# Kernel optimization log

Hardware: AMD Instinct MI355X
Metric: run time of the kernel (lower is better)

Reference implementation:

```python
import jax, jax.numpy as jnp
import numpy as np
import math

N_HEAD = 16

def _rope_tables(seq, dh, dtype):
    inv_freq = 1.0 / (10000.0 ** (jnp.arange(0, dh, 2, dtype=jnp.float32) / dh))
    angle = jnp.arange(seq, dtype=jnp.float32)[:, None] * inv_freq[None, :]  # [S, dh/2]
    sin = jnp.repeat(jnp.sin(angle), 2, axis=-1).astype(dtype)  # [S, dh]
    cos = jnp.repeat(jnp.cos(angle), 2, axis=-1).astype(dtype)
    return sin, cos

def _rotate_half(x):
    x_even = x[..., ::2]
    x_odd = x[..., 1::2]
    return jnp.stack([-x_odd, x_even], axis=-1).reshape(x.shape)

def _apply_rope(x, sin, cos):
    # x: [B, H, S, dh]; sin/cos: [S, dh]
    return x * cos[None, None] + _rotate_half(x) * sin[None, None]

def setup_inputs() -> dict:
    key = jax.random.key(0)
    ks = jax.random.split(key, 9)
    B, S, D = 2, 2048, 2048
    scale = 1.0 / math.sqrt(D)
    x = jax.random.normal(ks[0], (B, S, D), dtype=jnp.float32)
    wq = jax.random.normal(ks[1], (D, D), dtype=jnp.float32) * scale
    wk = jax.random.normal(ks[2], (D, D), dtype=jnp.float32) * scale
    wv = jax.random.normal(ks[3], (D, D), dtype=jnp.float32) * scale
    wo = jax.random.normal(ks[4], (D, D), dtype=jnp.float32) * scale
    bq = jnp.zeros((D,), jnp.float32)
    bk = jnp.zeros((D,), jnp.float32)
    bv = jnp.zeros((D,), jnp.float32)
    bo = jnp.zeros((D,), jnp.float32)
    # causal mask: True = masked (strict upper triangle)
    mask = jnp.triu(jnp.ones((S, S), dtype=bool), k=1)[None, None]  # [1,1,S,S]
    return {"x": x, "wq": wq, "bq": bq, "wk": wk, "bk": bk, "wv": wv, "bv": bv,
            "wo": wo, "bo": bo, "mask": mask}

def reference(x, wq, bq, wk, bk, wv, bv, wo, bo, mask):
    B, S, D = x.shape
    H = N_HEAD
    dh = D // H
    # projections (torch Linear: x @ W.T + b)
    q = (x @ wq.T + bq).reshape(B, S, H, dh).transpose(0, 2, 1, 3)  # [B,H,S,dh]
    k = (x @ wk.T + bk).reshape(B, S, H, dh).transpose(0, 2, 1, 3)
    v = (x @ wv.T + bv).reshape(B, S, H, dh).transpose(0, 2, 1, 3)
    sin, cos = _rope_tables(S, dh, x.dtype)
    q = _apply_rope(q, sin, cos)
    k = _apply_rope(k, sin, cos)
    scores = jnp.einsum('bhqd,bhkd->bhqk', q, k) / math.sqrt(dh)
    scores = jnp.where(mask, -jnp.inf, scores)
    attn = jax.nn.softmax(scores, axis=-1)
    attn = jnp.nan_to_num(attn, nan=0.0)
    out = jnp.einsum('bhqk,bhkd->bhqd', attn, v)  # [B,H,S,dh]
    out = out.transpose(0, 2, 1, 3).reshape(B, S, D)
    return out @ wo.T + bo
```

## Files before the change

### kernel.cpp

```cpp
#include <hip/hip_runtime.h>
#include <math.h>


typedef _Float16 half8 __attribute__((ext_vector_type(8)));
typedef _Float16 half4v __attribute__((ext_vector_type(4)));
typedef float f32x4 __attribute__((ext_vector_type(4)));

__device__ __forceinline__ void gl_lds16(const void* g, void* l) {
  __builtin_amdgcn_global_load_lds(
      (const __attribute__((address_space(1))) unsigned int*)g,
      (__attribute__((address_space(3))) unsigned int*)l, 16, 0, 0);
}

__global__ void cast_f32_f16(const float* __restrict__ src, _Float16* __restrict__ dst, int n4) {
  int i = blockIdx.x * blockDim.x + threadIdx.x;
  if (i >= n4) return;
  float4 v = reinterpret_cast<const float4*>(src)[i];
  half4v o;
  o[0] = (_Float16)v.x; o[1] = (_Float16)v.y; o[2] = (_Float16)v.z; o[3] = (_Float16)v.w;
  reinterpret_cast<half4v*>(dst)[i] = o;
}

__global__ void cast_w(const float* __restrict__ w0, const float* __restrict__ w1,
                       const float* __restrict__ w2, const float* __restrict__ w3,
                       _Float16* __restrict__ wdst) {
  const float* s = blockIdx.y == 0 ? w0 : blockIdx.y == 1 ? w1 : blockIdx.y == 2 ? w2 : w3;
  int i = blockIdx.x * blockDim.x + threadIdx.x;
  float4 v = reinterpret_cast<const float4*>(s)[i];
  half4v o;
  o[0] = (_Float16)v.x; o[1] = (_Float16)v.y; o[2] = (_Float16)v.z; o[3] = (_Float16)v.w;
  reinterpret_cast<half4v*>(wdst)[(size_t)blockIdx.y * 1048576 + i] = o;
}

template <bool OUT_F32>
__global__ __launch_bounds__(512, 2) void gemm_bt256(
    const _Float16* __restrict__ A,
    const _Float16* __restrict__ B,
    const float* __restrict__ b0, const float* __restrict__ b1,
    const float* __restrict__ b2,
    void* __restrict__ Cout,
    int M, int N, int K) {
  __shared__ _Float16 As[2][16384];
  __shared__ _Float16 Bs[2][16384];
  const int bm = blockIdx.y * 256, bn = blockIdx.x * 256;
  const int tid = threadIdx.x;
  const int wave = tid >> 6, lane = tid & 63;
  const int quad = lane >> 4, l16 = lane & 15;
  const int wm = (wave >> 2) * 128, wn = (wave & 3) * 64;

  const int srow = tid >> 3;
  const int sx = (tid & 7) ^ (srow & 7);
  const _Float16* Ag = A + (size_t)(bm + srow) * K + sx * 8;
  const _Float16* Bg[4];
#pragma unroll
  for (int c = 0; c < 4; ++c) {
    int r = (((c * 2 + (srow >> 5)) & 3) << 6) + ((c >> 1) << 5) + (srow & 31);
    Bg[c] = B + (size_t)(bn + r) * K + sx * 8;
  }

#define STAGE_A(buf, R, kt) \
  gl_lds16(Ag + (size_t)(R) * K + (kt) * 64, &As[buf][(R) * 64 + tid * 8])
#define STAGE_B(buf, c, kt) \
  gl_lds16(Bg[c] + (kt) * 64, &Bs[buf][(c) * 4096 + tid * 8])

  const int axor = l16 & 7;
  const int sl0 = ((0 + quad) ^ axor) * 8;
  const int sl1 = ((4 + quad) ^ axor) * 8;
  const int aoff = (wm + l16) * 64;
  const int q4 = (wn >> 6) * 32;

#define RD_A(i, kk) \
  (*reinterpret_cast<const half8*>(&As[cur][aoff + (i) * 1024 + ((kk) ? sl1 : sl0)]))
#define RD_B(j, kk) \
  (*reinterpret_cast<const half8*>( \
      &Bs[cur][((((j) >> 1) * 128 + q4 + ((j) & 1) * 16 + l16)) * 64 + ((kk) ? sl1 : sl0)]))

  f32x4 acc[8][4];
#pragma unroll
  for (int i = 0; i < 8; ++i)
#pragma unroll
    for (int j = 0; j < 4; ++j) acc[i][j] = f32x4{0.f, 0.f, 0.f, 0.f};

  half8 a[4][2], b[4][2];
  const int NT = K >> 6;

  STAGE_A(0, 0, 0); STAGE_A(0, 128, 0);
  STAGE_B(0, 0, 0); STAGE_B(0, 1, 0);
  STAGE_B(0, 2, 0); STAGE_B(0, 3, 0);
  STAGE_A(0, 64, 0); STAGE_A(0, 192, 0);
  if (NT > 1) {
    STAGE_A(1, 0, 1); STAGE_A(1, 128, 1);
    STAGE_B(1, 0, 1); STAGE_B(1, 1, 1);
    STAGE_B(1, 2, 1); STAGE_B(1, 3, 1);
    asm volatile("s_waitcnt vmcnt(6)");
  } else {
    asm volatile("s_waitcnt vmcnt(0)");
  }
  __builtin_amdgcn_s_barrier();

  for (int t = 0; t < NT; ++t) {
    const int cur = t & 1, nxt = cur ^ 1;
    const bool pf1 = (t + 1 < NT);
    const bool pf2 = (t + 2 < NT);

#pragma unroll
    for (int i = 0; i < 4; ++i) {
      a[i][0] = RD_A(i, 0); a[i][1] = RD_A(i, 1);
    }
#pragma unroll
    for (int j = 0; j < 2; ++j) {
      b[j][0] = RD_B(j, 0); b[j][1] = RD_B(j, 1);
    }
    if (pf1) { STAGE_A(nxt, 64, t + 1); STAGE_A(nxt, 192, t + 1); }
    __builtin_amdgcn_s_barrier();
    __builtin_amdgcn_s_setprio(1);
#pragma unroll
    for (int i = 0; i < 4; ++i)
#pragma unroll
      for (int j = 0; j < 2; ++j) {
        acc[i][j] = __builtin_amdgcn_mfma_f32_16x16x32_f16(a[i][0], b[j][0], acc[i][j], 0, 0, 0);
        acc[i][j] = __builtin_amdgcn_mfma_f32_16x16x32_f16(a[i][1], b[j][1], acc[i][j], 0, 0, 0);
      }
    __builtin_amdgcn_s_setprio(0);
    __builtin_amdgcn_s_barrier();

#pragma unroll
    for (int j = 2; j < 4; ++j) {
      b[j][0] = RD_B(j, 0); b[j][1] = RD_B(j, 1);
    }
    if (pf2) { STAGE_A(cur, 0, t + 2); STAGE_A(cur, 128, t + 2); }
    __builtin_amdgcn_s_barrier();
    __builtin_amdgcn_s_setprio(1);
#pragma unroll
    for (int i = 0; i < 4; ++i)
#pragma unroll
      for (int j = 2; j < 4; ++j) {
        acc[i][j] = __builtin_amdgcn_mfma_f32_16x16x32_f16(a[i][0], b[j][0], acc[i][j], 0, 0, 0);
        acc[i][j] = __builtin_amdgcn_mfma_f32_16x16x32_f16(a[i][1], b[j][1], acc[i][j], 0, 0, 0);
      }
    __builtin_amdgcn_s_setprio(0);
    __builtin_amdgcn_s_barrier();

#pragma unroll
    for (int i = 0; i < 4; ++i) {
      a[i][0] = RD_A(i + 4, 0); a[i][1] = RD_A(i + 4, 1);
    }
    if (pf2) { STAGE_B(cur, 0, t + 2); STAGE_B(cur, 1, t + 2); }
    __builtin_amdgcn_s_barrier();
    __builtin_amdgcn_s_setprio(1);
#pragma unroll
    for (int i = 0; i < 4; ++i)
#pragma unroll
      for (int j = 0; j < 2; ++j) {
        acc[i + 4][j] = __builtin_amdgcn_mfma_f32_16x16x32_f16(a[i][0], b[j][0], acc[i + 4][j], 0, 0, 0);
        acc[i + 4][j] = __builtin_amdgcn_mfma_f32_16x16x32_f16(a[i][1], b[j][1], acc[i + 4][j], 0, 0, 0);
      }
    __builtin_amdgcn_s_setprio(0);
    __builtin_amdgcn_s_barrier();

    if (pf2) { STAGE_B(cur, 2, t + 2); STAGE_B(cur, 3, t + 2); }
    __builtin_amdgcn_s_barrier();
    __builtin_amdgcn_s_setprio(1);
#pragma unroll
    for (int i = 0; i < 4; ++i)
#pragma unroll
      for (int j = 2; j < 4; ++j) {
        acc[i + 4][j] = __builtin_amdgcn_mfma_f32_16x16x32_f16(a[i][0], b[j][0], acc[i + 4][j], 0, 0, 0);
        acc[i + 4][j] = __builtin_amdgcn_mfma_f32_16x16x32_f16(a[i][1], b[j][1], acc[i + 4][j], 0, 0, 0);
      }
    __builtin_amdgcn_s_setprio(0);
    if (pf2)
      asm volatile("s_waitcnt vmcnt(6)");
    else
      asm volatile("s_waitcnt vmcnt(0)");
    __builtin_amdgcn_s_barrier();
  }

#pragma unroll
  for (int j = 0; j < 4; ++j) {
    const int gc = bn + wn + j * 16 + l16;
    const float* bp = (gc < 2048) ? b0 : (gc < 4096 ? b1 : b2);
    const float bz = bp[gc & 2047];
#pragma unroll
    for (int i = 0; i < 8; ++i) {
#pragma unroll
      for (int r = 0; r < 4; ++r) {
        const int gr = bm + wm + i * 16 + quad * 4 + r;
        float v = acc[i][j][r] + bz;
        if (OUT_F32)
          reinterpret_cast<float*>(Cout)[(size_t)gr * N + gc] = v;
        else
          reinterpret_cast<_Float16*>(Cout)[(size_t)gr * N + gc] = (_Float16)v;
      }
    }
  }
#undef STAGE_A
#undef STAGE_B
#undef RD_A
#undef RD_B
}

__global__ void rope_inplace(_Float16* __restrict__ qkv, int ngroups) {
  int idx = blockIdx.x * blockDim.x + threadIdx.x;
  if (idx >= ngroups) return;
  int m = idx >> 8;
  int g = idx & 255;
  int s = m & 2047;
  const float scale = 0.088388347648318447f;
  size_t base = (size_t)m * 6144 + g * 8;
  half8 qv = *reinterpret_cast<const half8*>(qkv + base);
  half8 kv = *reinterpret_cast<const half8*>(qkv + base + 2048);
  half8 qo, ko;
#pragma unroll
  for (int j = 0; j < 4; ++j) {
    int i = (g * 4 + j) & 63;
    float ang = (float)s * exp2f(-0.2076205059304601f * (float)i);
    float sn, cs;
    __sincosf(ang, &sn, &cs);
    float e = (float)qv[j * 2], o = (float)qv[j * 2 + 1];
    qo[j * 2]     = (_Float16)((e * cs - o * sn) * scale);
    qo[j * 2 + 1] = (_Float16)((o * cs + e * sn) * scale);
    e = (float)kv[j * 2]; o = (float)kv[j * 2 + 1];
    ko[j * 2]     = (_Float16)(e * cs - o * sn);
    ko[j * 2 + 1] = (_Float16)(o * cs + e * sn);
  }
  *reinterpret_cast<half8*>(qkv + base) = qo;
  *reinterpret_cast<half8*>(qkv + base + 2048) = ko;
}

__global__ __launch_bounds__(256) void transpose_v(const _Float16* __restrict__ qkv,
                                                   _Float16* __restrict__ vt) {
  __shared__ _Float16 t[64][72];
  const int s0 = blockIdx.x * 64;
  const int d0 = blockIdx.y * 64;
  const int bh = blockIdx.z;
  const int b = bh >> 4, h = bh & 15;
  const int tid = threadIdx.x;
#pragma unroll
  for (int p = 0; p < 2; ++p) {
    int chunk = p * 256 + tid;
    int r = chunk >> 3, c8 = (chunk & 7) * 8;
    *reinterpret_cast<half8*>(&t[r][c8]) = *reinterpret_cast<const half8*>(
        &qkv[(size_t)(b * 2048 + s0 + r) * 6144 + 4096 + h * 128 + d0 + c8]);
  }
  __syncthreads();
#pragma unroll
  for (int p = 0; p < 2; ++p) {
    int chunk = p * 256 + tid;
    int dr = chunk >> 3, c8 = (chunk & 7) * 8;
    half8 o;
#pragma unroll
    for (int j = 0; j < 8; ++j) o[j] = t[c8 + j][dr];
    *reinterpret_cast<half8*>(&vt[(size_t)(bh * 128 + d0 + dr) * 2048 + s0 + c8]) = o;
  }
}

__global__ __launch_bounds__(256, 2) void attn_kernel(
    const _Float16* __restrict__ QKV,
    const _Float16* __restrict__ VT,
    _Float16* __restrict__ ctx) {
  constexpr int LD = 6144, S = 2048;
  __shared__ _Float16 Ks[2][8192];
  __shared__ _Float16 Vs[2][8192];
  __shared__ _Float16 P[4][16][80];
  const int bid = blockIdx.x;
  const int bh = bid & 31;
  const int idx = (bid >> 5) & 7;
  const int qb = (bid >> 8) ? idx : 15 - idx;
  const int b = bh >> 4, h = bh & 15;
  const int tid = threadIdx.x;
  const int wv = tid >> 6, lane = tid & 63;
  const int quad = lane >> 4, l16 = lane & 15;
  const int q0 = qb * 128 + wv * 16;
  const int NJ = 2 * qb + 2;

  const _Float16* qp0 = QKV + (size_t)(b * S + q0 + l16) * LD + h * 128;
  half8 aq0[4], aq1[4];
#pragma unroll
  for (int ks = 0; ks < 4; ++ks) {
    aq0[ks] = *reinterpret_cast<const half8*>(qp0 + ks * 32 + quad * 8);
    aq1[ks] = *reinterpret_cast<const half8*>(qp0 + (size_t)64 * LD + ks * 32 + quad * 8);
  }

  const _Float16* gk[4];
  const _Float16* gv[4];
  int lofs[4];
#pragma unroll
  for (int p = 0; p < 4; ++p) {
    int c = p * 256 + tid;
    int cs = c ^ ((c >> 3) & 7);
    int cl16 = cs & 15, cqd = (cs >> 4) & 3;
    int cks = (cs >> 6) & 3, cf = cs >> 8;
    gk[p] = QKV + (size_t)(b * S + cf * 16 + cl16) * LD + 2048 + h * 128 + cks * 32 + cqd * 8;
    int ckv = (cs >> 6) & 1, ct = cs >> 7;
    gv[p] = VT + (size_t)(bh * 128 + ct * 16 + cl16) * S + ckv * 32 + cqd * 8;
    lofs[p] = c * 8;
  }

  const int kofs = (l16 >> 3) * 64 + (((l16 & 7) ^ (quad * 2 + (l16 >> 3)))) * 8;

  f32x4 acc0[8], acc1[8];
#pragma unroll
  for (int t = 0; t < 8; ++t) {
    acc0[t] = f32x4{0.f, 0.f, 0.f, 0.f};
    acc1[t] = f32x4{0.f, 0.f, 0.f, 0.f};
  }
  f32x4 lacc0 = f32x4{0.f, 0.f, 0.f, 0.f};
  f32x4 lacc1 = f32x4{0.f, 0.f, 0.f, 0.f};

  half8 ones;
#pragma unroll
  for (int j = 0; j < 8; ++j) ones[j] = (_Float16)1.0f;

#pragma unroll
  for (int p = 0; p < 4; ++p) gl_lds16(gk[p], &Ks[0][lofs[p]]);
#pragma unroll
  for (int p = 0; p < 4; ++p) gl_lds16(gv[p], &Vs[0][lofs[p]]);

  for (int j = 0; j < NJ; ++j) {
    __syncthreads();
    const int cur = j & 1;
    if (j + 1 < NJ) {
      const size_t ko = (size_t)(j + 1) * 64 * LD;
      const int vo = (j + 1) * 64;
#pragma unroll
      for (int p = 0; p < 4; ++p) gl_lds16(gk[p] + ko, &Ks[cur ^ 1][lofs[p]]);
#pragma unroll
      for (int p = 0; p < 4; ++p) gl_lds16(gv[p] + vo, &Vs[cur ^ 1][lofs[p]]);
    }
    const bool h0 = (j < NJ - 1);
    f32x4 sf0[4], sf1[4];
#pragma unroll
    for (int f = 0; f < 4; ++f) {
      sf0[f] = f32x4{0.f, 0.f, 0.f, 0.f};
      sf1[f] = f32x4{0.f, 0.f, 0.f, 0.f};
    }
#pragma unroll
    for (int f = 0; f < 4; ++f)
#pragma unroll
      for (int ks = 0; ks < 4; ++ks) {
        half8 bk = *reinterpret_cast<const half8*>(&Ks[cur][((f * 4 + ks) * 4 + quad) * 128 + kofs]);
        sf0[f] = __builtin_amdgcn_mfma_f32_16x16x32_f16(aq0[ks], bk, sf0[f], 0, 0, 0);
        sf1[f] = __builtin_amdgcn_mfma_f32_16x16x32_f16(aq1[ks], bk, sf1[f], 0, 0, 0);
      }
    if (j == NJ - 2) {
#pragma unroll
      for (int f = 0; f < 4; ++f) {
        const int key = j * 64 + f * 16 + l16;
#pragma unroll
        for (int r = 0; r < 4; ++r)
          sf0[f][r] = (key <= q0 + quad * 4 + r) ? sf0[f][r] : -1e30f;
      }
    }
    if (j == NJ - 1) {
#pragma unroll
      for (int f = 0; f < 4; ++f) {
        const int key = j * 64 + f * 16 + l16;
#pragma unroll
        for (int r = 0; r < 4; ++r)
          sf1[f][r] = (key <= q0 + 64 + quad * 4 + r) ? sf1[f][r] : -1e30f;
      }
    }
    half8 pa0a, pa0b, pa1a, pa1b;
    if (h0) {
#pragma unroll
      for (int f = 0; f < 4; ++f)
#pragma unroll
        for (int r = 0; r < 4; ++r)
          P[wv][quad * 4 + r][f * 16 + l16] = (_Float16)__expf(sf0[f][r] - 5.0f);
      pa0a = *reinterpret_cast<const half8*>(&P[wv][l16][quad * 8]);
      pa0b = *reinterpret_cast<const half8*>(&P[wv][l16][32 + quad * 8]);
    }
#pragma unroll
    for (int f = 0; f < 4; ++f)
#pragma unroll
      for (int r = 0; r < 4; ++r)
        P[wv][quad * 4 + r][f * 16 + l16] = (_Float16)__expf(sf1[f][r] - 5.0f);
    pa1a = *reinterpret_cast<const half8*>(&P[wv][l16][quad * 8]);
    pa1b = *reinterpret_cast<const half8*>(&P[wv][l16][32 + quad * 8]);
#pragma unroll
    for (int t = 0; t < 8; ++t) {
      half8 bv0 = *reinterpret_cast<const half8*>(&Vs[cur][((t * 2 + 0) * 4 + quad) * 128 + kofs]);
      half8 bv1 = *reinterpret_cast<const half8*>(&Vs[cur][((t * 2 + 1) * 4 + quad) * 128 + kofs]);
      if (h0) {
        acc0[t] = __builtin_amdgcn_mfma_f32_16x16x32_f16(pa0a, bv0, acc0[t], 0, 0, 0);
        acc0[t] = __builtin_amdgcn_mfma_f32_16x16x32_f16(pa0b, bv1, acc0[t], 0, 0, 0);
      }
      acc1[t] = __builtin_amdgcn_mfma_f32_16x16x32_f16(pa1a, bv0, acc1[t], 0, 0, 0);
      acc1[t] = __builtin_amdgcn_mfma_f32_16x16x32_f16(pa1b, bv1, acc1[t], 0, 0, 0);
    }
    if (h0) {
      lacc0 = __builtin_amdgcn_mfma_f32_16x16x32_f16(pa0a, ones, lacc0, 0, 0, 0);
      lacc0 = __builtin_amdgcn_mfma_f32_16x16x32_f16(pa0b, ones, lacc0, 0, 0, 0);
    }
    lacc1 = __builtin_amdgcn_mfma_f32_16x16x32_f16(pa1a, ones, lacc1, 0, 0, 0);
    lacc1 = __builtin_amdgcn_mfma_f32_16x16x32_f16(pa1b, ones, lacc1, 0, 0, 0);
  }

  float inv0[4], inv1[4];
#pragma unroll
  for (int r = 0; r < 4; ++r) {
    inv0[r] = 1.0f / lacc0[r];
    inv1[r] = 1.0f / lacc1[r];
  }
#pragma unroll
  for (int t = 0; t < 8; ++t)
#pragma unroll
    for (int r = 0; r < 4; ++r) {
      const int row0 = q0 + quad * 4 + r;
      ctx[(size_t)(b * S + row0) * 2048 + h * 128 + t * 16 + l16] =
          (_Float16)(acc0[t][r] * inv0[r]);
      ctx[(size_t)(b * S + row0 + 64) * 2048 + h * 128 + t * 16 + l16] =
          (_Float16)(acc1[t][r] * inv1[r]);
    }
}

extern "C" void kernel_launch(void* const* d_in, const int* in_sizes, int n_in,
                              void* d_out, int out_size, void* d_ws, size_t ws_size,
                              hipStream_t stream) {
  const float* x  = (const float*)d_in[0];
  const float* wq = (const float*)d_in[1];
  const float* bq = (const float*)d_in[2];
  const float* wk = (const float*)d_in[3];
  const float* bk = (const float*)d_in[4];
  const float* wv = (const float*)d_in[5];
  const float* bv = (const float*)d_in[6];
  const float* wo = (const float*)d_in[7];
  const float* bo = (const float*)d_in[8];

  _Float16* W      = (_Float16*)d_ws;
  _Float16* xh     = W;
  _Float16* wqkvh  = xh + 8388608;
  _Float16* woh    = wqkvh + 12582912;
  _Float16* qkvlin = woh + 4194304;
  _Float16* vT     = xh;
  _Float16* ctx    = wqkvh;

  cast_f32_f16<<<8192, 256, 0, stream>>>(x, xh, 2097152);
  cast_w<<<dim3(4096, 4), 256, 0, stream>>>(wq, wk, wv, wo, wqkvh);

  gemm_bt256<false><<<dim3(24, 16), 512, 0, stream>>>(xh, wqkvh, bq, bk, bv, qkvlin,
                                                      4096, 6144, 2048);

  rope_inplace<<<4096, 256, 0, stream>>>(qkvlin, 1048576);
  transpose_v<<<dim3(32, 2, 32), 256, 0, stream>>>(qkvlin, vT);
  attn_kernel<<<512, 256, 0, stream>>>(qkvlin, vT, ctx);

  gemm_bt256<true><<<dim3(8, 16), 512, 0, stream>>>(ctx, woh, bo, bo, bo, (float*)d_out,
                                                    4096, 2048, 2048);
}
```

Measured before the change: 438.8 us.

## Fuse RoPE into QKV GEMM epilogue and retile output projection GEMM

Specializes the QKV GEMM with compile-time K/N and a 2x-unrolled k-loop so buffer indices are constants, and applies RoPE plus the query scale in its epilogue using lane shuffles, removing the separate rope_inplace pass over Q/K. The output projection gets its own 256x128 tile kernel, doubling the grid from 128 to 256 blocks to fill more CUs. The epilogue now does per-element sincos work and the new tile has lower arithmetic intensity per block.

```diff
diff --git a/kernel.cpp b/kernel.cpp
--- a/kernel.cpp
+++ b/kernel.cpp
@@ -32,14 +32,15 @@
   reinterpret_cast<half4v*>(wdst)[(size_t)blockIdx.y * 1048576 + i] = o;
 }
 
-template <bool OUT_F32>
-__global__ __launch_bounds__(512, 2) void gemm_bt256(
+__global__ __launch_bounds__(512, 2) void gemm_qkv(
     const _Float16* __restrict__ A,
     const _Float16* __restrict__ B,
     const float* __restrict__ b0, const float* __restrict__ b1,
     const float* __restrict__ b2,
-    void* __restrict__ Cout,
-    int M, int N, int K) {
+    _Float16* __restrict__ Cout) {
+  constexpr int K = 2048;
+  constexpr int N = 6144;
+  constexpr int NT = K >> 6;
   __shared__ _Float16 As[2][16384];
   __shared__ _Float16 Bs[2][16384];
   const int bm = blockIdx.y * 256, bn = blockIdx.x * 256;
@@ -82,115 +83,107 @@
     for (int j = 0; j < 4; ++j) acc[i][j] = f32x4{0.f, 0.f, 0.f, 0.f};
 
   half8 a[4][2], b[4][2];
-  const int NT = K >> 6;
 
   STAGE_A(0, 0, 0); STAGE_A(0, 128, 0);
   STAGE_B(0, 0, 0); STAGE_B(0, 1, 0);
   STAGE_B(0, 2, 0); STAGE_B(0, 3, 0);
   STAGE_A(0, 64, 0); STAGE_A(0, 192, 0);
-  if (NT > 1) {
-    STAGE_A(1, 0, 1); STAGE_A(1, 128, 1);
-    STAGE_B(1, 0, 1); STAGE_B(1, 1, 1);
-    STAGE_B(1, 2, 1); STAGE_B(1, 3, 1);
-    asm volatile("s_waitcnt vmcnt(6)");
-  } else {
-    asm volatile("s_waitcnt vmcnt(0)");
-  }
+  STAGE_A(1, 0, 1); STAGE_A(1, 128, 1);
+  STAGE_B(1, 0, 1); STAGE_B(1, 1, 1);
+  STAGE_B(1, 2, 1); STAGE_B(1, 3, 1);
+  asm volatile("s_waitcnt vmcnt(6)");
   __builtin_amdgcn_s_barrier();
 
-  for (int t = 0; t < NT; ++t) {
-    const int cur = t & 1, nxt = cur ^ 1;
-    const bool pf1 = (t + 1 < NT);
-    const bool pf2 = (t + 2 < NT);
-
-#pragma unroll
-    for (int i = 0; i < 4; ++i) {
-      a[i][0] = RD_A(i, 0); a[i][1] = RD_A(i, 1);
-    }
-#pragma unroll
-    for (int j = 0; j < 2; ++j) {
-      b[j][0] = RD_B(j, 0); b[j][1] = RD_B(j, 1);
-    }
-    if (pf1) { STAGE_A(nxt, 64, t + 1); STAGE_A(nxt, 192, t + 1); }
-    __builtin_amdgcn_s_barrier();
-    __builtin_amdgcn_s_setprio(1);
-#pragma unroll
-    for (int i = 0; i < 4; ++i)
-#pragma unroll
-      for (int j = 0; j < 2; ++j) {
-        acc[i][j] = __builtin_amdgcn_mfma_f32_16x16x32_f16(a[i][0], b[j][0], acc[i][j], 0, 0, 0);
-        acc[i][j] = __builtin_amdgcn_mfma_f32_16x16x32_f16(a[i][1], b[j][1], acc[i][j], 0, 0, 0);
-      }
-    __builtin_amdgcn_s_setprio(0);
-    __builtin_amdgcn_s_barrier();
-
-#pragma unroll
-    for (int j = 2; j < 4; ++j) {
-      b[j][0] = RD_B(j, 0); b[j][1] = RD_B(j, 1);
-    }
-    if (pf2) { STAGE_A(cur, 0, t + 2); STAGE_A(cur, 128, t + 2); }
-    __builtin_amdgcn_s_barrier();
-    __builtin_amdgcn_s_setprio(1);
-#pragma unroll
-    for (int i = 0; i < 4; ++i)
-#pragma unroll
-      for (int j = 2; j < 4; ++j) {
-        acc[i][j] = __builtin_amdgcn_mfma_f32_16x16x32_f16(a[i][0], b[j][0], acc[i][j], 0, 0, 0);
-        acc[i][j] = __builtin_amdgcn_mfma_f32_16x16x32_f16(a[i][1], b[j][1], acc[i][j], 0, 0, 0);
-      }
-    __builtin_amdgcn_s_setprio(0);
-    __builtin_amdgcn_s_barrier();
-
-#pragma unroll
-    for (int i = 0; i < 4; ++i) {
-      a[i][0] = RD_A(i + 4, 0); a[i][1] = RD_A(i + 4, 1);
-    }
-    if (pf2) { STAGE_B(cur, 0, t + 2); STAGE_B(cur, 1, t + 2); }
-    __builtin_amdgcn_s_barrier();
-    __builtin_amdgcn_s_setprio(1);
-#pragma unroll
-    for (int i = 0; i < 4; ++i)
-#pragma unroll
-      for (int j = 0; j < 2; ++j) {
-        acc[i + 4][j] = __builtin_amdgcn_mfma_f32_16x16x32_f16(a[i][0], b[j][0], acc[i + 4][j], 0, 0, 0);
-        acc[i + 4][j] = __builtin_amdgcn_mfma_f32_16x16x32_f16(a[i][1], b[j][1], acc[i + 4][j], 0, 0, 0);
-      }
-    __builtin_amdgcn_s_setprio(0);
-    __builtin_amdgcn_s_barrier();
-
-    if (pf2) { STAGE_B(cur, 2, t + 2); STAGE_B(cur, 3, t + 2); }
-    __builtin_amdgcn_s_barrier();
-    __builtin_amdgcn_s_setprio(1);
-#pragma unroll
-    for (int i = 0; i < 4; ++i)
-#pragma unroll
-      for (int j = 2; j < 4; ++j) {
-        acc[i + 4][j] = __builtin_amdgcn_mfma_f32_16x16x32_f16(a[i][0], b[j][0], acc[i + 4][j], 0, 0, 0);
-        acc[i + 4][j] = __builtin_amdgcn_mfma_f32_16x16x32_f16(a[i][1], b[j][1], acc[i + 4][j], 0, 0, 0);
-      }
-    __builtin_amdgcn_s_setprio(0);
-    if (pf2)
-      asm volatile("s_waitcnt vmcnt(6)");
-    else
-      asm volatile("s_waitcnt vmcnt(0)");
-    __builtin_amdgcn_s_barrier();
-  }
-
+#define KSTEP_BODY                                                             \
+  {                                                                            \
+    const bool pf1 = (t + 1 < NT);                                             \
+    const bool pf2 = (t + 2 < NT);                                             \
+    _Pragma("unroll") for (int i = 0; i < 4; ++i) {                            \
+      a[i][0] = RD_A(i, 0); a[i][1] = RD_A(i, 1);                              \
+    }                                                                          \
+    _Pragma("unroll") for (int j = 0; j < 2; ++j) {                            \
+      b[j][0] = RD_B(j, 0); b[j][1] = RD_B(j, 1);                              \
+    }                                                                          \
+    if (pf1) { STAGE_A(nxt, 64, t + 1); STAGE_A(nxt, 192, t + 1); }            \
+    __builtin_amdgcn_s_barrier();                                              \
+    __builtin_amdgcn_s_setprio(1);                                             \
+    _Pragma("unroll") for (int i = 0; i < 4; ++i)                              \
+      _Pragma("unroll") for (int j = 0; j < 2; ++j) {                          \
+        acc[i][j] = __builtin_amdgcn_mfma_f32_16x16x32_f16(a[i][0], b[j][0], acc[i][j], 0, 0, 0); \
+        acc[i][j] = __builtin_amdgcn_mfma_f32_16x16x32_f16(a[i][1], b[j][1], acc[i][j], 0, 0, 0); \
+      }                                                                        \
+    __builtin_amdgcn_s_setprio(0);                                             \
+    __builtin_amdgcn_s_barrier();                                              \
+    _Pragma("unroll") for (int j = 2; j < 4; ++j) {                            \
+      b[j][0] = RD_B(j, 0); b[j][1] = RD_B(j, 1);                              \
+    }                                                                          \
+    if (pf2) { STAGE_A(cur, 0, t + 2); STAGE_A(cur, 128, t + 2); }             \
+    __builtin_amdgcn_s_barrier();                                              \
+    __builtin_amdgcn_s_setprio(1);                                             \
+    _Pragma("unroll") for (int i = 0; i < 4; ++i)                              \
+      _Pragma("unroll") for (int j = 2; j < 4; ++j) {                          \
+        acc[i][j] = __builtin_amdgcn_mfma_f32_16x16x32_f16(a[i][0], b[j][0], acc[i][j], 0, 0, 0); \
+        acc[i][j] = __builtin_amdgcn_mfma_f32_16x16x32_f16(a[i][1], b[j][1], acc[i][j], 0, 0, 0); \
+      }                                                                        \
+    __builtin_amdgcn_s_setprio(0);                                             \
+    __builtin_amdgcn_s_barrier();                                              \
+    _Pragma("unroll") for (int i = 0; i < 4; ++i) {                            \
+      a[i][0] = RD_A(i + 4, 0); a[i][1] = RD_A(i + 4, 1);                      \
+    }                                                                          \
+    if (pf2) { STAGE_B(cur, 0, t + 2); STAGE_B(cur, 1, t + 2); }               \
+    __builtin_amdgcn_s_barrier();                                              \
+    __builtin_amdgcn_s_setprio(1);                                             \
+    _Pragma("unroll") for (int i = 0; i < 4; ++i)                              \
+      _Pragma("unroll") for (int j = 0; j < 2; ++j) {                          \
+        acc[i + 4][j] = __builtin_amdgcn_mfma_f32_16x16x32_f16(a[i][0], b[j][0], acc[i + 4][j], 0, 0, 0); \
+        acc[i + 4][j] = __builtin_amdgcn_mfma_f32_16x16x32_f16(a[i][1], b[j][1], acc[i + 4][j], 0, 0, 0); \
+      }                                                                        \
+    __builtin_amdgcn_s_setprio(0);                                             \
+    __builtin_amdgcn_s_barrier();                                              \
+    if (pf2) { STAGE_B(cur, 2, t + 2); STAGE_B(cur, 3, t + 2); }               \
+    __builtin_amdgcn_s_barrier();                                              \
+    __builtin_amdgcn_s_setprio(1);                                             \
+    _Pragma("unroll") for (int i = 0; i < 4; ++i)                              \
+      _Pragma("unroll") for (int j = 2; j < 4; ++j) {                          \
+        acc[i + 4][j] = __builtin_amdgcn_mfma_f32_16x16x32_f16(a[i][0], b[j][0], acc[i + 4][j], 0, 0, 0); \
+        acc[i + 4][j] = __builtin_amdgcn_mfma_f32_16x16x32_f16(a[i][1], b[j][1], acc[i + 4][j], 0, 0, 0); \
+      }                                                                        \
+    __builtin_amdgcn_s_setprio(0);                                             \
+    if (pf2) asm volatile("s_waitcnt vmcnt(6)");                               \
+    else     asm volatile("s_waitcnt vmcnt(0)");                               \
+    __builtin_amdgcn_s_barrier();                                              \
+  }
+
+  for (int tt = 0; tt < NT; tt += 2) {
+    { constexpr int cur = 0, nxt = 1; const int t = tt;     KSTEP_BODY }
+    { constexpr int cur = 1, nxt = 0; const int t = tt + 1; KSTEP_BODY }
+  }
+
+  const int region = (bn + wn) >> 11;
+  const float ropescale = 0.088388347648318447f;
 #pragma unroll
   for (int j = 0; j < 4; ++j) {
     const int gc = bn + wn + j * 16 + l16;
-    const float* bp = (gc < 2048) ? b0 : (gc < 4096 ? b1 : b2);
+    const float* bp = (region == 0) ? b0 : (region == 1 ? b1 : b2);
     const float bz = bp[gc & 2047];
+    const int fi = (gc >> 1) & 63;
+    const float fr = exp2f(-0.2076205059304601f * (float)fi);
+    const bool isodd = (gc & 1) != 0;
 #pragma unroll
     for (int i = 0; i < 8; ++i) {
 #pragma unroll
       for (int r = 0; r < 4; ++r) {
         const int gr = bm + wm + i * 16 + quad * 4 + r;
         float v = acc[i][j][r] + bz;
-        if (OUT_F32)
-          reinterpret_cast<float*>(Cout)[(size_t)gr * N + gc] = v;
-        else
-          reinterpret_cast<_Float16*>(Cout)[(size_t)gr * N + gc] = (_Float16)v;
+        if (region < 2) {
+          const float p = __shfl_xor(v, 1);
+          const int s = gr & 2047;
+          float sn, cs;
+          __sincosf((float)s * fr, &sn, &cs);
+          v = isodd ? (v * cs + p * sn) : (v * cs - p * sn);
+          if (region == 0) v *= ropescale;
+        }
+        Cout[(size_t)gr * N + gc] = (_Float16)v;
       }
     }
   }
@@ -198,34 +191,139 @@
 #undef STAGE_B
 #undef RD_A
 #undef RD_B
-}
-
-__global__ void rope_inplace(_Float16* __restrict__ qkv, int ngroups) {
-  int idx = blockIdx.x * blockDim.x + threadIdx.x;
-  if (idx >= ngroups) return;
-  int m = idx >> 8;
-  int g = idx & 255;
-  int s = m & 2047;
-  const float scale = 0.088388347648318447f;
-  size_t base = (size_t)m * 6144 + g * 8;
-  half8 qv = *reinterpret_cast<const half8*>(qkv + base);
-  half8 kv = *reinterpret_cast<const half8*>(qkv + base + 2048);
-  half8 qo, ko;
-#pragma unroll
-  for (int j = 0; j < 4; ++j) {
-    int i = (g * 4 + j) & 63;
-    float ang = (float)s * exp2f(-0.2076205059304601f * (float)i);
-    float sn, cs;
-    __sincosf(ang, &sn, &cs);
-    float e = (float)qv[j * 2], o = (float)qv[j * 2 + 1];
-    qo[j * 2]     = (_Float16)((e * cs - o * sn) * scale);
-    qo[j * 2 + 1] = (_Float16)((o * cs + e * sn) * scale);
-    e = (float)kv[j * 2]; o = (float)kv[j * 2 + 1];
-    ko[j * 2]     = (_Float16)(e * cs - o * sn);
-    ko[j * 2 + 1] = (_Float16)(o * cs + e * sn);
-  }
-  *reinterpret_cast<half8*>(qkv + base) = qo;
-  *reinterpret_cast<half8*>(qkv + base + 2048) = ko;
+#undef KSTEP_BODY
+}
+
+__global__ __launch_bounds__(512, 2) void gemm_out(
+    const _Float16* __restrict__ A,
+    const _Float16* __restrict__ B,
+    const float* __restrict__ bias,
+    float* __restrict__ Cout) {
+  constexpr int K = 2048;
+  constexpr int N = 2048;
+  constexpr int NT = K >> 6;
+  __shared__ _Float16 As[2][16384];
+  __shared__ _Float16 Bs[2][8192];
+  const int bm = blockIdx.y * 256, bn = blockIdx.x * 128;
+  const int tid = threadIdx.x;
+  const int wave = tid >> 6, lane = tid & 63;
+  const int quad = lane >> 4, l16 = lane & 15;
+  const int wm = (wave >> 2) * 128, wq = wave & 3;
+
+  const int srow = tid >> 3;
+  const int sx = (tid & 7) ^ (srow & 7);
+  const _Float16* Ag = A + (size_t)(bm + srow) * K + sx * 8;
+  const _Float16* Bg[2];
+#pragma unroll
+  for (int c = 0; c < 2; ++c)
+    Bg[c] = B + (size_t)(bn + (srow >> 4) * 32 + c * 16 + (srow & 15)) * K + sx * 8;
+
+#define STAGE_A(buf, R, kt) \
+  gl_lds16(Ag + (size_t)(R) * K + (kt) * 64, &As[buf][(R) * 64 + tid * 8])
+#define STAGE_B(buf, c, kt) \
+  gl_lds16(Bg[c] + (kt) * 64, &Bs[buf][(c) * 4096 + tid * 8])
+
+  const int axor = l16 & 7;
+  const int sl0 = ((0 + quad) ^ axor) * 8;
+  const int sl1 = ((4 + quad) ^ axor) * 8;
+  const int aoff = (wm + l16) * 64;
+
+#define RD_A(i, kk) \
+  (*reinterpret_cast<const half8*>(&As[cur][aoff + (i) * 1024 + ((kk) ? sl1 : sl0)]))
+#define RD_B(j, kk) \
+  (*reinterpret_cast<const half8*>( \
+      &Bs[cur][((j) * 64 + wq * 16 + l16) * 64 + ((kk) ? sl1 : sl0)]))
+
+  f32x4 acc[8][2];
+#pragma unroll
+  for (int i = 0; i < 8; ++i)
+#pragma unroll
+    for (int j = 0; j < 2; ++j) acc[i][j] = f32x4{0.f, 0.f, 0.f, 0.f};
+
+  half8 a[4][2], b[2][2];
+
+  STAGE_A(0, 0, 0); STAGE_A(0, 128, 0);
+  STAGE_B(0, 0, 0); STAGE_B(0, 1, 0);
+  STAGE_A(0, 64, 0); STAGE_A(0, 192, 0);
+  STAGE_A(1, 0, 1); STAGE_A(1, 128, 1);
+  STAGE_B(1, 0, 1); STAGE_B(1, 1, 1);
+  STAGE_A(1, 64, 1); STAGE_A(1, 192, 1);
+  asm volatile("s_waitcnt vmcnt(6)");
+  __builtin_amdgcn_s_barrier();
+
+#define OSTEP_BODY                                                             \
+  {                                                                            \
+    const bool pf2 = (t + 2 < NT);                                             \
+    _Pragma("unroll") for (int i = 0; i < 4; ++i) {                            \
+      a[i][0] = RD_A(i, 0); a[i][1] = RD_A(i, 1);                              \
+    }                                                                          \
+    b[0][0] = RD_B(0, 0); b[0][1] = RD_B(0, 1);                                \
+    __builtin_amdgcn_s_barrier();                                              \
+    __builtin_amdgcn_s_setprio(1);                                             \
+    _Pragma("unroll") for (int i = 0; i < 4; ++i) {                            \
+      acc[i][0] = __builtin_amdgcn_mfma_f32_16x16x32_f16(a[i][0], b[0][0], acc[i][0], 0, 0, 0); \
+      acc[i][0] = __builtin_amdgcn_mfma_f32_16x16x32_f16(a[i][1], b[0][1], acc[i][0], 0, 0, 0); \
+    }                                                                          \
+    __builtin_amdgcn_s_setprio(0);                                             \
+    __builtin_amdgcn_s_barrier();                                              \
+    b[1][0] = RD_B(1, 0); b[1][1] = RD_B(1, 1);                                \
+    if (pf2) { STAGE_A(cur, 0, t + 2); STAGE_A(cur, 128, t + 2); }             \
+    __builtin_amdgcn_s_barrier();                                              \
+    __builtin_amdgcn_s_setprio(1);                                             \
+    _Pragma("unroll") for (int i = 0; i < 4; ++i) {                            \
+      acc[i][1] = __builtin_amdgcn_mfma_f32_16x16x32_f16(a[i][0], b[1][0], acc[i][1], 0, 0, 0); \
+      acc[i][1] = __builtin_amdgcn_mfma_f32_16x16x32_f16(a[i][1], b[1][1], acc[i][1], 0, 0, 0); \
+    }                                                                          \
+    __builtin_amdgcn_s_setprio(0);                                             \
+    __builtin_amdgcn_s_barrier();                                              \
+    _Pragma("unroll") for (int i = 0; i < 4; ++i) {                            \
+      a[i][0] = RD_A(i + 4, 0); a[i][1] = RD_A(i + 4, 1);                      \
+    }                                                                          \
+    if (pf2) { STAGE_B(cur, 0, t + 2); STAGE_B(cur, 1, t + 2); }               \
+    __builtin_amdgcn_s_barrier();                                              \
+    __builtin_amdgcn_s_setprio(1);                                             \
+    _Pragma("unroll") for (int i = 0; i < 4; ++i) {                            \
+      acc[i + 4][0] = __builtin_amdgcn_mfma_f32_16x16x32_f16(a[i][0], b[0][0], acc[i + 4][0], 0, 0, 0); \
+      acc[i + 4][0] = __builtin_amdgcn_mfma_f32_16x16x32_f16(a[i][1], b[0][1], acc[i + 4][0], 0, 0, 0); \
+    }                                                                          \
+    __builtin_amdgcn_s_setprio(0);                                             \
+    __builtin_amdgcn_s_barrier();                                              \
+    if (pf2) { STAGE_A(cur, 64, t + 2); STAGE_A(cur, 192, t + 2); }            \
+    __builtin_amdgcn_s_barrier();                                              \
+    __builtin_amdgcn_s_setprio(1);                                             \
+    _Pragma("unroll") for (int i = 0; i < 4; ++i) {                            \
+      acc[i + 4][1] = __builtin_amdgcn_mfma_f32_16x16x32_f16(a[i][0], b[1][0], acc[i + 4][1], 0, 0, 0); \
+      acc[i + 4][1] = __builtin_amdgcn_mfma_f32_16x16x32_f16(a[i][1], b[1][1], acc[i + 4][1], 0, 0, 0); \
+    }                                                                          \
+    __builtin_amdgcn_s_setprio(0);                                             \
+    if (pf2) asm volatile("s_waitcnt vmcnt(6)");                               \
+    else     asm volatile("s_waitcnt vmcnt(0)");                               \
+    __builtin_amdgcn_s_barrier();                                              \
+  }
+
+  for (int tt = 0; tt < NT; tt += 2) {
+    { constexpr int cur = 0; const int t = tt;     OSTEP_BODY }
+    { constexpr int cur = 1; const int t = tt + 1; OSTEP_BODY }
+  }
+
+#pragma unroll
+  for (int j = 0; j < 2; ++j) {
+    const int gc = bn + wq * 32 + j * 16 + l16;
+    const float bz = bias[gc & 2047];
+#pragma unroll
+    for (int i = 0; i < 8; ++i) {
+#pragma unroll
+      for (int r = 0; r < 4; ++r) {
+        const int gr = bm + wm + i * 16 + quad * 4 + r;
+        Cout[(size_t)gr * N + gc] = acc[i][j][r] + bz;
+      }
+    }
+  }
+#undef STAGE_A
+#undef STAGE_B
+#undef RD_A
+#undef RD_B
+#undef OSTEP_BODY
 }
 
 __global__ __launch_bounds__(256) void transpose_v(const _Float16* __restrict__ qkv,
@@ -439,13 +537,10 @@
   cast_f32_f16<<<8192, 256, 0, stream>>>(x, xh, 2097152);
   cast_w<<<dim3(4096, 4), 256, 0, stream>>>(wq, wk, wv, wo, wqkvh);
 
-  gemm_bt256<false><<<dim3(24, 16), 512, 0, stream>>>(xh, wqkvh, bq, bk, bv, qkvlin,
-                                                      4096, 6144, 2048);
-
-  rope_inplace<<<4096, 256, 0, stream>>>(qkvlin, 1048576);
+  gemm_qkv<<<dim3(24, 16), 512, 0, stream>>>(xh, wqkvh, bq, bk, bv, qkvlin);
+
   transpose_v<<<dim3(32, 2, 32), 256, 0, stream>>>(qkvlin, vT);
   attn_kernel<<<512, 256, 0, stream>>>(qkvlin, vT, ctx);
 
-  gemm_bt256<true><<<dim3(8, 16), 512, 0, stream>>>(ctx, woh, bo, bo, bo, (float*)d_out,
-                                                    4096, 2048, 2048);
-}
+  gemm_out<<<dim3(16, 16), 512, 0, stream>>>(ctx, woh, bo, (float*)d_out);
+}
```

After: 422.5 us. 3.7% less time.
